# Kernel tuning notes

Measured on AMD Instinct MI355X. Metric: run time of the kernel, lower is better.

## Reference

```python
import jax, jax.numpy as jnp
import numpy as np

CE_W, DICE_W, BD_W = 1.0, 3.0, 2.0   # combined-loss lambdas
BPW = 10.0                            # boundary pixel weight
SMOOTH = 1e-6                         # dice smoothing
# cv2.getStructuringElement(cv2.MORPH_ELLIPSE, (5,5))
ELLIPSE5 = np.array([[0,0,1,0,0],
                     [1,1,1,1,1],
                     [1,1,1,1,1],
                     [1,1,1,1,1],
                     [0,0,1,0,0]], dtype=bool)


def setup_inputs() -> dict:
    key = jax.random.key(0)
    k1, k2 = jax.random.split(key)
    B, C, H, W = 8, 8, 512, 1024
    pred = jax.random.normal(k1, (B, C, H, W), dtype=jnp.float32)
    target = jax.random.randint(k2, (B, H, W), 0, C).astype(jnp.int32)
    return {"pred": pred, "target": target}


def _morph(mask, is_dilate):
    """Grayscale dilate/erode with 5x5 ellipse SE (matches cv2 default border:
    padding value never wins the max/min)."""
    pad_val = 0 if is_dilate else jnp.iinfo(jnp.int32).max
    p = jnp.pad(mask, ((0, 0), (2, 2), (2, 2)), constant_values=pad_val)
    H, W = mask.shape[1], mask.shape[2]
    out = None
    for dy in range(5):
        for dx in range(5):
            if not ELLIPSE5[dy, dx]:
                continue
            s = p[:, dy:dy + H, dx:dx + W]
            if out is None:
                out = s
            else:
                out = jnp.maximum(out, s) if is_dilate else jnp.minimum(out, s)
    return out


def reference(pred, target):
    B, C, H, W = pred.shape
    logp = jax.nn.log_softmax(pred, axis=1)                         # (B,C,H,W)
    # per-pixel cross entropy
    ce_map = -jnp.take_along_axis(logp, target[:, None], axis=1)[:, 0]  # (B,H,W)
    ce = ce_map.mean()
    # dice over softmax probs vs one-hot target
    probs = jnp.exp(logp)
    onehot = jax.nn.one_hot(target, C, dtype=pred.dtype, axis=1)    # (B,C,H,W)
    inter = jnp.sum(probs * onehot, axis=(2, 3))                    # (B,C)
    card = jnp.sum(probs, axis=(2, 3)) + jnp.sum(onehot, axis=(2, 3))
    dice = 1.0 - jnp.mean((2.0 * inter + SMOOTH) / (card + SMOOTH))
    # boundary mask = morphological gradient of the label map
    t = target.astype(jnp.int32)
    boundary = _morph(t, True) - _morph(t, False)                   # (B,H,W)
    wmap = jnp.where(boundary > 0, jnp.float32(BPW), jnp.float32(1.0))
    bd = jnp.mean(ce_map * wmap)
    return CE_W * ce + DICE_W * dice + BD_W * bd
```

## Files before the change

kernel.cpp:

```cpp
#include <hip/hip_runtime.h>
#include <math.h>

constexpr int B = 8, C = 8, H = 512, W = 1024;
constexpr int RH = 4;
constexpr int NT = 256;
constexpr float BPW = 10.0f;
constexpr float SMOOTH = 1e-6f;

constexpr int ACC_N = 2 + 3 * B * C;

__device__ __forceinline__ unsigned win_or5(unsigned lo, unsigned mid, unsigned hi) {
    unsigned long long a = ((unsigned long long)mid << 32) | lo;
    unsigned long long b = ((unsigned long long)hi << 32) | mid;
    return (unsigned)(a >> 16) | (unsigned)(a >> 24) | mid |
           (unsigned)(b >> 8) | (unsigned)(b >> 16);
}

__device__ __forceinline__ unsigned pack_row(const int* __restrict__ tb, int gh, int gc) {
    if (gh < 0 || gh >= H || gc < 0 || gc >= W) return 0u;
    const int4 t4 = *reinterpret_cast<const int4*>(tb + (size_t)gh * W + gc);
    return (1u << t4.x) | ((1u << t4.y) << 8) | ((1u << t4.z) << 16) | ((1u << t4.w) << 24);
}

__global__ __launch_bounds__(NT, 4)
void loss_main(const float* __restrict__ pred, const int* __restrict__ target,
               float* __restrict__ acc) {
    __shared__ float sred[4][26];

    const int tid = threadIdx.x;
    const int h0 = blockIdx.x * RH;
    const int b  = blockIdx.y;
    const int gc = tid * 4;

    const int* tb = target + (size_t)b * H * W;
    const size_t plane = (size_t)H * W;
    const float* pb = pred + (size_t)b * C * plane;

    float4 x[C];
    {
        const size_t p0 = (size_t)h0 * W + gc;
#pragma unroll
        for (int c = 0; c < C; ++c)
            x[c] = *reinterpret_cast<const float4*>(pb + c * plane + p0);
    }

    unsigned cw0 = pack_row(tb, h0 - 2, gc);
    unsigned cw1 = pack_row(tb, h0 - 1, gc);
    unsigned cw2 = pack_row(tb, h0,     gc);
    unsigned cw3 = pack_row(tb, h0 + 1, gc);
    unsigned lw0 = pack_row(tb, h0 - 1, gc - 4);
    unsigned lw1 = pack_row(tb, h0,     gc - 4);
    unsigned rw0 = pack_row(tb, h0 - 1, gc + 4);
    unsigned rw1 = pack_row(tb, h0,     gc + 4);

    float ce_s = 0.f, bd_s = 0.f;
    float p_s[C], in_s[C];
    unsigned cnt_lo = 0u, cnt_hi = 0u;
#pragma unroll
    for (int c = 0; c < C; ++c) { p_s[c] = 0.f; in_s[c] = 0.f; }

#pragma unroll
    for (int s = 0; s < RH; ++s) {
        const int y = h0 + s;

        const unsigned cw4 = pack_row(tb, y + 2, gc);
        const unsigned lw2 = pack_row(tb, y + 1, gc - 4);
        const unsigned rw2 = pack_row(tb, y + 1, gc + 4);

        float4 xn[C];
        if (s < RH - 1) {
            const size_t pn = (size_t)(y + 1) * W + gc;
#pragma unroll
            for (int c = 0; c < C; ++c)
                xn[c] = *reinterpret_cast<const float4*>(pb + c * plane + pn);
        }

        const unsigned bm4 = win_or5(lw0 | lw1 | lw2, cw1 | cw2 | cw3, rw0 | rw1 | rw2)
                             | cw0 | cw4;
        const unsigned cmid = cw2;

#pragma unroll
        for (int j = 0; j < 4; ++j) {
            const float x0 = (j==0)?x[0].x:(j==1)?x[0].y:(j==2)?x[0].z:x[0].w;
            const float x1 = (j==0)?x[1].x:(j==1)?x[1].y:(j==2)?x[1].z:x[1].w;
            const float x2 = (j==0)?x[2].x:(j==1)?x[2].y:(j==2)?x[2].z:x[2].w;
            const float x3 = (j==0)?x[3].x:(j==1)?x[3].y:(j==2)?x[3].z:x[3].w;
            const float x4 = (j==0)?x[4].x:(j==1)?x[4].y:(j==2)?x[4].z:x[4].w;
            const float x5 = (j==0)?x[5].x:(j==1)?x[5].y:(j==2)?x[5].z:x[5].w;
            const float x6 = (j==0)?x[6].x:(j==1)?x[6].y:(j==2)?x[6].z:x[6].w;
            const float x7 = (j==0)?x[7].x:(j==1)?x[7].y:(j==2)?x[7].z:x[7].w;

            const float e0 = __expf(x0), e1 = __expf(x1), e2 = __expf(x2), e3 = __expf(x3);
            const float e4 = __expf(x4), e5 = __expf(x5), e6 = __expf(x6), e7 = __expf(x7);
            const float sum = ((e0 + e1) + (e2 + e3)) + ((e4 + e5) + (e6 + e7));

            const unsigned cm  = (cmid >> (8 * j)) & 0xFFu;
            const unsigned bmj = (bm4  >> (8 * j)) & 0xFFu;
            const int t = 31 - __clz(cm);

            float xt = x0;
            xt = (t == 1) ? x1 : xt;  xt = (t == 2) ? x2 : xt;
            xt = (t == 3) ? x3 : xt;  xt = (t == 4) ? x4 : xt;
            xt = (t == 5) ? x5 : xt;  xt = (t == 6) ? x6 : xt;
            xt = (t == 7) ? x7 : xt;

            const float ce = __logf(sum) - xt;
            const float wgt = (bmj & (bmj - 1u)) ? BPW : 1.f;
            ce_s += ce;
            bd_s = fmaf(ce, wgt, bd_s);

            const unsigned inc = 1u << ((t & 3) << 3);
            cnt_lo += (t < 4) ? inc : 0u;
            cnt_hi += (t < 4) ? 0u : inc;

            const float invs = 1.f / sum;
            const float p0 = e0 * invs, p1 = e1 * invs, p2 = e2 * invs, p3 = e3 * invs;
            const float p4 = e4 * invs, p5 = e5 * invs, p6 = e6 * invs, p7 = e7 * invs;
            p_s[0] += p0; p_s[1] += p1; p_s[2] += p2; p_s[3] += p3;
            p_s[4] += p4; p_s[5] += p5; p_s[6] += p6; p_s[7] += p7;
            in_s[0] += (t == 0) ? p0 : 0.f;  in_s[1] += (t == 1) ? p1 : 0.f;
            in_s[2] += (t == 2) ? p2 : 0.f;  in_s[3] += (t == 3) ? p3 : 0.f;
            in_s[4] += (t == 4) ? p4 : 0.f;  in_s[5] += (t == 5) ? p5 : 0.f;
            in_s[6] += (t == 6) ? p6 : 0.f;  in_s[7] += (t == 7) ? p7 : 0.f;
        }

        cw0 = cw1; cw1 = cw2; cw2 = cw3; cw3 = cw4;
        lw0 = lw1; lw1 = lw2;
        rw0 = rw1; rw1 = rw2;
        if (s < RH - 1) {
#pragma unroll
            for (int c = 0; c < C; ++c) x[c] = xn[c];
        }
    }

    float vals[26];
    vals[0] = ce_s; vals[1] = bd_s;
#pragma unroll
    for (int c = 0; c < C; ++c) {
        vals[2 + c]  = p_s[c];
        vals[10 + c] = in_s[c];
        vals[18 + c] = (float)(((c < 4 ? (cnt_lo >> (8 * c)) : (cnt_hi >> (8 * (c - 4))))) & 0xFFu);
    }
#pragma unroll
    for (int k = 0; k < 26; ++k) {
        float v = vals[k];
#pragma unroll
        for (int off = 32; off > 0; off >>= 1) v += __shfl_down(v, off, 64);
        vals[k] = v;
    }
    const int lane = tid & 63, wid = tid >> 6;
    if (lane == 0) {
#pragma unroll
        for (int k = 0; k < 26; ++k) sred[wid][k] = vals[k];
    }
    __syncthreads();
    if (tid < 26) {
        const float v = sred[0][tid] + sred[1][tid] + sred[2][tid] + sred[3][tid];
        int gi;
        if (tid == 0)       gi = 0;
        else if (tid == 1)  gi = 1;
        else if (tid < 10)  gi = 2 + b * C + (tid - 2);
        else if (tid < 18)  gi = 2 + B * C + b * C + (tid - 10);
        else                gi = 2 + 2 * B * C + b * C + (tid - 18);
        atomicAdd(&acc[gi], v);
    }
}

__global__ void loss_final(const float* __restrict__ acc, float* __restrict__ out) {
    const int i = threadIdx.x;
    const float psum  = acc[2 + i];
    const float inter = acc[2 + B * C + i];
    const float cnt   = acc[2 + 2 * B * C + i];
    float d = (2.f * inter + SMOOTH) / (psum + cnt + SMOOTH);
#pragma unroll
    for (int off = 32; off > 0; off >>= 1) d += __shfl_down(d, off, 64);
    if (i == 0) {
        const float N = (float)B * H * W;
        const float ce = acc[0] / N;
        const float bd = acc[1] / N;
        const float dice = 1.f - d / (float)(B * C);
        out[0] = 1.0f * ce + 3.0f * dice + 2.0f * bd;
    }
}

extern "C" void kernel_launch(void* const* d_in, const int* in_sizes, int n_in,
                              void* d_out, int out_size, void* d_ws, size_t ws_size,
                              hipStream_t stream) {
    const float* pred = (const float*)d_in[0];
    const int* target = (const int*)d_in[1];
    float* acc = (float*)d_ws;
    float* out = (float*)d_out;

    hipMemsetAsync(acc, 0, ACC_N * sizeof(float), stream);

    dim3 grid(H / RH, B);
    loss_main<<<grid, NT, 0, stream>>>(pred, target, acc);
    loss_final<<<1, 64, 0, stream>>>(acc, out);
}
```

Baseline: 256.4 us.

## Halve rows per block, preload both rows, compute CE from log-prob

Each block now handles 2 rows instead of 4. All target rows and both pred rows are loaded up front instead of being streamed row by row. The reciprocal uses the hardware rcp builtin, and cross-entropy is computed as -log(p_t) rather than log(sum)-x_t. Per-class counts are packed into 4-bit nibbles of one register, and the occupancy hint in launch_bounds is dropped. The aim is more memory-level parallelism and fewer ALU ops, at the cost of twice as many blocks, atomics and reductions, more redundant halo loads of the target, and slightly different numerics.

Result: faster. 211.1 us (-17.7%).

```diff
diff --git a/kernel.cpp b/kernel.cpp
--- a/kernel.cpp
+++ b/kernel.cpp
@@ -2,7 +2,7 @@
 #include <math.h>
 
 constexpr int B = 8, C = 8, H = 512, W = 1024;
-constexpr int RH = 4;
+constexpr int RH = 2;
 constexpr int NT = 256;
 constexpr float BPW = 10.0f;
 constexpr float SMOOTH = 1e-6f;
@@ -22,7 +22,7 @@
     return (1u << t4.x) | ((1u << t4.y) << 8) | ((1u << t4.z) << 16) | ((1u << t4.w) << 24);
 }
 
-__global__ __launch_bounds__(NT, 4)
+__global__ __launch_bounds__(NT)
 void loss_main(const float* __restrict__ pred, const int* __restrict__ target,
                float* __restrict__ acc) {
     __shared__ float sred[4][26];
@@ -34,50 +34,43 @@
 
     const int* tb = target + (size_t)b * H * W;
     const size_t plane = (size_t)H * W;
-    const float* pb = pred + (size_t)b * C * plane;
+    const float* pb = pred + (size_t)b * C * plane + (size_t)h0 * W + gc;
 
-    float4 x[C];
-    {
-        const size_t p0 = (size_t)h0 * W + gc;
+    const unsigned c0 = pack_row(tb, h0 - 2, gc);
+    const unsigned c1 = pack_row(tb, h0 - 1, gc);
+    const unsigned c2 = pack_row(tb, h0,     gc);
+    const unsigned c3 = pack_row(tb, h0 + 1, gc);
+    const unsigned c4 = pack_row(tb, h0 + 2, gc);
+    const unsigned c5 = pack_row(tb, h0 + 3, gc);
+    const unsigned l0 = pack_row(tb, h0 - 1, gc - 4);
+    const unsigned l1 = pack_row(tb, h0,     gc - 4);
+    const unsigned l2 = pack_row(tb, h0 + 1, gc - 4);
+    const unsigned l3 = pack_row(tb, h0 + 2, gc - 4);
+    const unsigned r0 = pack_row(tb, h0 - 1, gc + 4);
+    const unsigned r1 = pack_row(tb, h0,     gc + 4);
+    const unsigned r2 = pack_row(tb, h0 + 1, gc + 4);
+    const unsigned r3 = pack_row(tb, h0 + 2, gc + 4);
+
+    float4 xa[C], xb[C];
 #pragma unroll
-        for (int c = 0; c < C; ++c)
-            x[c] = *reinterpret_cast<const float4*>(pb + c * plane + p0);
-    }
-
-    unsigned cw0 = pack_row(tb, h0 - 2, gc);
-    unsigned cw1 = pack_row(tb, h0 - 1, gc);
-    unsigned cw2 = pack_row(tb, h0,     gc);
-    unsigned cw3 = pack_row(tb, h0 + 1, gc);
-    unsigned lw0 = pack_row(tb, h0 - 1, gc - 4);
-    unsigned lw1 = pack_row(tb, h0,     gc - 4);
-    unsigned rw0 = pack_row(tb, h0 - 1, gc + 4);
-    unsigned rw1 = pack_row(tb, h0,     gc + 4);
+    for (int c = 0; c < C; ++c) xa[c] = *reinterpret_cast<const float4*>(pb + c * plane);
+#pragma unroll
+    for (int c = 0; c < C; ++c) xb[c] = *reinterpret_cast<const float4*>(pb + c * plane + W);
 
     float ce_s = 0.f, bd_s = 0.f;
     float p_s[C], in_s[C];
-    unsigned cnt_lo = 0u, cnt_hi = 0u;
+    unsigned cnt = 0u;
 #pragma unroll
     for (int c = 0; c < C; ++c) { p_s[c] = 0.f; in_s[c] = 0.f; }
 
+    const unsigned bmA = win_or5(l0 | l1 | l2, c1 | c2 | c3, r0 | r1 | r2) | c0 | c4;
+    const unsigned bmB = win_or5(l1 | l2 | l3, c2 | c3 | c4, r1 | r2 | r3) | c1 | c5;
+
 #pragma unroll
-    for (int s = 0; s < RH; ++s) {
-        const int y = h0 + s;
-
-        const unsigned cw4 = pack_row(tb, y + 2, gc);
-        const unsigned lw2 = pack_row(tb, y + 1, gc - 4);
-        const unsigned rw2 = pack_row(tb, y + 1, gc + 4);
-
-        float4 xn[C];
-        if (s < RH - 1) {
-            const size_t pn = (size_t)(y + 1) * W + gc;
-#pragma unroll
-            for (int c = 0; c < C; ++c)
-                xn[c] = *reinterpret_cast<const float4*>(pb + c * plane + pn);
-        }
-
-        const unsigned bm4 = win_or5(lw0 | lw1 | lw2, cw1 | cw2 | cw3, rw0 | rw1 | rw2)
-                             | cw0 | cw4;
-        const unsigned cmid = cw2;
+    for (int s = 0; s < 2; ++s) {
+        const float4* x = (s == 0) ? xa : xb;
+        const unsigned cmid = (s == 0) ? c2 : c3;
+        const unsigned bm4  = (s == 0) ? bmA : bmB;
 
 #pragma unroll
         for (int j = 0; j < 4; ++j) {
@@ -93,43 +86,33 @@
             const float e0 = __expf(x0), e1 = __expf(x1), e2 = __expf(x2), e3 = __expf(x3);
             const float e4 = __expf(x4), e5 = __expf(x5), e6 = __expf(x6), e7 = __expf(x7);
             const float sum = ((e0 + e1) + (e2 + e3)) + ((e4 + e5) + (e6 + e7));
+            const float invs = __builtin_amdgcn_rcpf(sum);
 
             const unsigned cm  = (cmid >> (8 * j)) & 0xFFu;
             const unsigned bmj = (bm4  >> (8 * j)) & 0xFFu;
             const int t = 31 - __clz(cm);
 
-            float xt = x0;
-            xt = (t == 1) ? x1 : xt;  xt = (t == 2) ? x2 : xt;
-            xt = (t == 3) ? x3 : xt;  xt = (t == 4) ? x4 : xt;
-            xt = (t == 5) ? x5 : xt;  xt = (t == 6) ? x6 : xt;
-            xt = (t == 7) ? x7 : xt;
-
-            const float ce = __logf(sum) - xt;
-            const float wgt = (bmj & (bmj - 1u)) ? BPW : 1.f;
-            ce_s += ce;
-            bd_s = fmaf(ce, wgt, bd_s);
-
-            const unsigned inc = 1u << ((t & 3) << 3);
-            cnt_lo += (t < 4) ? inc : 0u;
-            cnt_hi += (t < 4) ? 0u : inc;
-
-            const float invs = 1.f / sum;
             const float p0 = e0 * invs, p1 = e1 * invs, p2 = e2 * invs, p3 = e3 * invs;
             const float p4 = e4 * invs, p5 = e5 * invs, p6 = e6 * invs, p7 = e7 * invs;
             p_s[0] += p0; p_s[1] += p1; p_s[2] += p2; p_s[3] += p3;
             p_s[4] += p4; p_s[5] += p5; p_s[6] += p6; p_s[7] += p7;
-            in_s[0] += (t == 0) ? p0 : 0.f;  in_s[1] += (t == 1) ? p1 : 0.f;
-            in_s[2] += (t == 2) ? p2 : 0.f;  in_s[3] += (t == 3) ? p3 : 0.f;
-            in_s[4] += (t == 4) ? p4 : 0.f;  in_s[5] += (t == 5) ? p5 : 0.f;
-            in_s[6] += (t == 6) ? p6 : 0.f;  in_s[7] += (t == 7) ? p7 : 0.f;
-        }
 
-        cw0 = cw1; cw1 = cw2; cw2 = cw3; cw3 = cw4;
-        lw0 = lw1; lw1 = lw2;
-        rw0 = rw1; rw1 = rw2;
-        if (s < RH - 1) {
-#pragma unroll
-            for (int c = 0; c < C; ++c) x[c] = xn[c];
+            const bool b0 = (t == 0), b1 = (t == 1), b2 = (t == 2), b3 = (t == 3);
+            const bool b4 = (t == 4), b5 = (t == 5), b6 = (t == 6), b7 = (t == 7);
+            in_s[0] += b0 ? p0 : 0.f;  in_s[1] += b1 ? p1 : 0.f;
+            in_s[2] += b2 ? p2 : 0.f;  in_s[3] += b3 ? p3 : 0.f;
+            in_s[4] += b4 ? p4 : 0.f;  in_s[5] += b5 ? p5 : 0.f;
+            in_s[6] += b6 ? p6 : 0.f;  in_s[7] += b7 ? p7 : 0.f;
+
+            float pt = p0;
+            pt = b1 ? p1 : pt;  pt = b2 ? p2 : pt;  pt = b3 ? p3 : pt;
+            pt = b4 ? p4 : pt;  pt = b5 ? p5 : pt;  pt = b6 ? p6 : pt;
+            pt = b7 ? p7 : pt;
+            const float l = __logf(pt);
+            const float wgt = (bmj & (bmj - 1u)) ? BPW : 1.f;
+            ce_s -= l;
+            bd_s = fmaf(-l, wgt, bd_s);
+            cnt += 1u << (t << 2);
         }
     }
 
@@ -139,7 +122,7 @@
     for (int c = 0; c < C; ++c) {
         vals[2 + c]  = p_s[c];
         vals[10 + c] = in_s[c];
-        vals[18 + c] = (float)(((c < 4 ? (cnt_lo >> (8 * c)) : (cnt_hi >> (8 * (c - 4))))) & 0xFFu);
+        vals[18 + c] = (float)((cnt >> (4 * c)) & 0xFu);
     }
 #pragma unroll
     for (int k = 0; k < 26; ++k) {
```
